# Optimization experiments

Measured on AMD Instinct MI355X. Metric: run time of the kernel, lower is better.

Reference implementation:

```python
import jax, jax.numpy as jnp
import numpy as np

C_PARAM = 2.0
EPS = 1e-05

def setup_inputs() -> dict:
    key = jax.random.key(0)
    x = jax.random.normal(key, (2048, 512, 7, 7), dtype=jnp.float32)
    return {"x": x}

def reference(x) -> jnp.ndarray:
    # y[n,c] = spatial mean over HW
    y = jnp.mean(x, axis=(2, 3))                      # [N, C]
    # per-sample channel stats (biased variance, matching mean(x^2)-mean^2)
    m = jnp.mean(y, axis=1, keepdims=True)            # [N, 1]
    mx2 = jnp.mean(y * y, axis=1, keepdims=True)      # [N, 1]
    var = jnp.maximum(mx2 - m * m, 0.0)
    inv_std = jax.lax.rsqrt(var + EPS)
    y_norm = (y - m) * inv_std                        # [N, C]
    gate = jnp.exp(-0.5 * C_PARAM * y_norm * y_norm)  # [N, C]
    return x * gate[:, :, None, None]
```

## Files before the change

kernel.cpp:

```cpp
#include <hip/hip_runtime.h>
#include <math.h>


#define NN 2048
#define CC 512
#define HW 49
#define CHCH 128
#define CHEL (CHCH * HW)
#define CHV4 (CHEL / 4)
#define NCHUNK (CC / CHCH)
#define EPS 1e-5f

__global__ __launch_bounds__(512, 4) void gate_kernel(const float* __restrict__ x,
                                                      float* __restrict__ out) {
    __shared__ float lds[CHEL];
    __shared__ float wsum[8];
    __shared__ float wsum2[8];
    __shared__ float s_m, s_inv;

    const int n = blockIdx.x;
    const int tid = threadIdx.x;
    const size_t nbase = (size_t)n * (CC * HW);

    float v[HW];

    const float4* __restrict__ xin4 = (const float4*)(x + nbase);
    for (int j = 0; j < NCHUNK; ++j) {
        for (int i = tid; i < CHV4; i += 512) {
            ((float4*)lds)[i] = xin4[j * CHV4 + i];
        }
        __syncthreads();
        if ((tid >> 7) == j) {
            const int base = (tid & (CHCH - 1)) * HW;
#pragma unroll
            for (int l = 0; l < HW; ++l) v[l] = lds[base + l];
        }
        __syncthreads();
    }

    float s = 0.0f;
#pragma unroll
    for (int l = 0; l < HW; ++l) s += v[l];
    const float y = s * (1.0f / (float)HW);

    float sum = y, sum2 = y * y;
#pragma unroll
    for (int off = 32; off > 0; off >>= 1) {
        sum  += __shfl_down(sum, off);
        sum2 += __shfl_down(sum2, off);
    }
    const int wave = tid >> 6;
    const int lane = tid & 63;
    if (lane == 0) { wsum[wave] = sum; wsum2[wave] = sum2; }
    __syncthreads();
    if (tid == 0) {
        float ts = 0.0f, ts2 = 0.0f;
#pragma unroll
        for (int w = 0; w < 8; ++w) { ts += wsum[w]; ts2 += wsum2[w]; }
        const float m = ts * (1.0f / (float)CC);
        float var = ts2 * (1.0f / (float)CC) - m * m;
        var = fmaxf(var, 0.0f);
        s_m = m;
        s_inv = rsqrtf(var + EPS);
    }
    __syncthreads();

    const float yn = (y - s_m) * s_inv;
    const float gate = expf(-yn * yn);

    float4* __restrict__ out4 = (float4*)(out + nbase);
    for (int j = 0; j < NCHUNK; ++j) {
        if ((tid >> 7) == j) {
            const int base = (tid & (CHCH - 1)) * HW;
#pragma unroll
            for (int l = 0; l < HW; ++l) lds[base + l] = v[l] * gate;
        }
        __syncthreads();
        for (int i = tid; i < CHV4; i += 512) {
            out4[j * CHV4 + i] = ((float4*)lds)[i];
        }
        __syncthreads();
    }
}

extern "C" void kernel_launch(void* const* d_in, const int* in_sizes, int n_in,
                              void* d_out, int out_size, void* d_ws, size_t ws_size,
                              hipStream_t stream) {
    const float* x = (const float*)d_in[0];
    float* out = (float*)d_out;
    gate_kernel<<<NN, 512, 0, stream>>>(x, out);
}
```

Baseline: 344.9 us.

## Split fused gate kernel into stats pass and streaming apply pass

Replaces the single fused kernel, which held each channel's 49 values in registers across the reduction, with two kernels. The first computes per-sample channel means and writes the gate vector to workspace. The second is a flat float4 elementwise kernel that rereads x and multiplies by the gate. This removes register pressure and staged LDS writeback in exchange for an extra full read of x and a second launch.

```diff
diff --git a/kernel.cpp b/kernel.cpp
--- a/kernel.cpp
+++ b/kernel.cpp
@@ -11,8 +11,8 @@
 #define NCHUNK (CC / CHCH)
 #define EPS 1e-5f
 
-__global__ __launch_bounds__(512, 4) void gate_kernel(const float* __restrict__ x,
-                                                      float* __restrict__ out) {
+__global__ __launch_bounds__(512) void stats_kernel(const float* __restrict__ x,
+                                                    float* __restrict__ gate) {
     __shared__ float lds[CHEL];
     __shared__ float wsum[8];
     __shared__ float wsum2[8];
@@ -21,10 +21,9 @@
     const int n = blockIdx.x;
     const int tid = threadIdx.x;
     const size_t nbase = (size_t)n * (CC * HW);
+    const float4* __restrict__ xin4 = (const float4*)(x + nbase);
 
-    float v[HW];
-
-    const float4* __restrict__ xin4 = (const float4*)(x + nbase);
+    float y = 0.0f;
     for (int j = 0; j < NCHUNK; ++j) {
         for (int i = tid; i < CHV4; i += 512) {
             ((float4*)lds)[i] = xin4[j * CHV4 + i];
@@ -32,16 +31,13 @@
         __syncthreads();
         if ((tid >> 7) == j) {
             const int base = (tid & (CHCH - 1)) * HW;
+            float s = 0.0f;
 #pragma unroll
-            for (int l = 0; l < HW; ++l) v[l] = lds[base + l];
+            for (int l = 0; l < HW; ++l) s += lds[base + l];
+            y = s * (1.0f / (float)HW);
         }
         __syncthreads();
     }
-
-    float s = 0.0f;
-#pragma unroll
-    for (int l = 0; l < HW; ++l) s += v[l];
-    const float y = s * (1.0f / (float)HW);
 
     float sum = y, sum2 = y * y;
 #pragma unroll
@@ -66,21 +62,27 @@
     __syncthreads();
 
     const float yn = (y - s_m) * s_inv;
-    const float gate = expf(-yn * yn);
+    gate[(size_t)n * CC + tid] = expf(-yn * yn);
+}
 
-    float4* __restrict__ out4 = (float4*)(out + nbase);
-    for (int j = 0; j < NCHUNK; ++j) {
-        if ((tid >> 7) == j) {
-            const int base = (tid & (CHCH - 1)) * HW;
-#pragma unroll
-            for (int l = 0; l < HW; ++l) lds[base + l] = v[l] * gate;
-        }
-        __syncthreads();
-        for (int i = tid; i < CHV4; i += 512) {
-            out4[j * CHV4 + i] = ((float4*)lds)[i];
-        }
-        __syncthreads();
-    }
+__global__ __launch_bounds__(256) void apply_kernel(const float* __restrict__ x,
+                                                    const float* __restrict__ gate,
+                                                    float* __restrict__ out) {
+    const unsigned i  = blockIdx.x * 256u + threadIdx.x;
+    const unsigned e0 = i * 4u;
+    const unsigned d0 = e0 / 49u;
+    const unsigned r0 = e0 - d0 * 49u;
+
+    const float4 v = ((const float4*)x)[i];
+    const float g0 = gate[d0];
+    const float g1 = (r0 >= 46u) ? gate[d0 + 1] : g0;
+
+    float4 o;
+    o.x = v.x * g0;
+    o.y = v.y * ((r0 >= 48u) ? g1 : g0);
+    o.z = v.z * ((r0 >= 47u) ? g1 : g0);
+    o.w = v.w * ((r0 >= 46u) ? g1 : g0);
+    ((float4*)out)[i] = o;
 }
 
 extern "C" void kernel_launch(void* const* d_in, const int* in_sizes, int n_in,
@@ -88,5 +90,10 @@
                               hipStream_t stream) {
     const float* x = (const float*)d_in[0];
     float* out = (float*)d_out;
-    gate_kernel<<<NN, 512, 0, stream>>>(x, out);
+    float* gate = (float*)d_ws;
+
+    stats_kernel<<<NN, 512, 0, stream>>>(x, gate);
+
+    const int total4 = NN * CC * HW / 4;
+    apply_kernel<<<total4 / 256, 256, 0, stream>>>(x, gate, out);
 }
```

Measured after the change: 375.1 us. 8.8% more time.
